# Kernel tuning notes

Hardware: AMD Instinct MI355X
Metric: run time of the kernel (lower is better)

The kernel has to match this reference:

```python
import jax, jax.numpy as jnp
import numpy as np

D_MODEL = 1024
D_HIDDEN = 4096
N_LATENTS = 64
D_LATENT = 1024
N_HEADS = 16
N_EXPERTS = 8
TOP_K = 2
B, T = 2, 2048
D_H = D_LATENT // N_HEADS  # 64


def setup_inputs() -> dict:
    key = jax.random.key(0)
    ks = jax.random.split(key, 16)
    x = jax.random.normal(ks[0], (B, T, D_MODEL), jnp.float32)
    # real RoPE cache (matches RoPE.build_rope_cache)
    half = D_H // 2
    inv_freq = 1.0 / (10000.0 ** (jnp.arange(half, dtype=jnp.float32) / half))
    ang = jnp.arange(T, dtype=jnp.float32)[:, None] * inv_freq[None, :]
    cos, sin = jnp.cos(ang), jnp.sin(ang)
    sL = D_LATENT ** -0.5
    sM = D_MODEL ** -0.5
    sH = D_HIDDEN ** -0.5
    def nrm(k, shape, sc):
        return jax.random.normal(k, shape, jnp.float32) * sc
    aks = jax.random.split(ks[1], 8)
    eks = jax.random.split(ks[2], 3)
    return {
        'x': x, 'cos': cos, 'sin': sin,
        'ln1_g': jnp.ones((D_MODEL,), jnp.float32), 'ln1_b': jnp.zeros((D_MODEL,), jnp.float32),
        'ln2_g': jnp.ones((D_MODEL,), jnp.float32), 'ln2_b': jnp.zeros((D_MODEL,), jnp.float32),
        'ln3_g': jnp.ones((D_MODEL,), jnp.float32), 'ln3_b': jnp.zeros((D_MODEL,), jnp.float32),
        'Lat': nrm(aks[0], (N_LATENTS, D_LATENT), sL),
        'Wq_lat': nrm(aks[1], (D_LATENT, D_LATENT), sL),
        'Wk_in': nrm(aks[2], (D_MODEL, D_LATENT), sM),
        'Wv_in': nrm(aks[3], (D_MODEL, D_LATENT), sM),
        'Wq_in': nrm(aks[4], (D_MODEL, D_LATENT), sM),
        'Wk_lat': nrm(aks[5], (D_LATENT, D_LATENT), sL),
        'Wv_lat': nrm(aks[6], (D_LATENT, D_LATENT), sL),
        'Wout_attn': nrm(aks[7], (D_LATENT, D_MODEL), sL),
        'router_W': nrm(ks[3], (D_MODEL, N_EXPERTS), sM),
        'router_b': jnp.zeros((N_EXPERTS,), jnp.float32),
        'expert_W': nrm(eks[0], (N_EXPERTS, D_MODEL, D_HIDDEN), sM),
        'expert_V': nrm(eks[1], (N_EXPERTS, D_MODEL, D_HIDDEN), sM),
        'expert_Wo': nrm(eks[2], (N_EXPERTS, D_HIDDEN, D_MODEL), sH),
        'lin_W': nrm(ks[4], (D_MODEL, D_MODEL), sM),
        'lin_b': jnp.zeros((D_MODEL,), jnp.float32),
    }


def _layernorm(x, g, b):
    mean = jnp.mean(x, axis=-1, keepdims=True)
    std = jnp.std(x, axis=-1, keepdims=True, ddof=1)  # torch std is unbiased
    return g * (x - mean) / (std + 1e-06) + b


def _split_heads(x):
    b, t, _ = x.shape
    return x.reshape(b, t, N_HEADS, D_H).transpose(0, 2, 1, 3)  # [b,h,t,dh]


def _merge_heads(x):
    b, h, t, dh = x.shape
    return x.transpose(0, 2, 1, 3).reshape(b, t, h * dh)


def _apply_rope(x, cos, sin):
    b, h, s, d = x.shape
    xr = x.reshape(b, h, s, d // 2, 2)
    x1, x2 = xr[..., 0], xr[..., 1]
    c = cos[:s][None, None]
    sn = sin[:s][None, None]
    o1 = x1 * c - x2 * sn
    o2 = x1 * sn + x2 * c
    return jnp.stack([o1, o2], axis=-1).reshape(b, h, s, d)


def _attn(Q, K, V):
    scores = jnp.einsum('bhqd,bhkd->bhqk', Q, K) / (D_H ** 0.5)
    w = jax.nn.softmax(scores, axis=-1)
    return jnp.einsum('bhqk,bhkd->bhqd', w, V)


def _mlha(x, cos, sin, Lat, Wq_lat, Wk_in, Wv_in, Wq_in, Wk_lat, Wv_lat, Wout_attn):
    b = x.shape[0]
    Lb = jnp.broadcast_to(Lat[None], (b, N_LATENTS, D_LATENT))
    Q = _split_heads(Lb @ Wq_lat)
    K = _apply_rope(_split_heads(x @ Wk_in), cos, sin)
    V = _split_heads(x @ Wv_in)
    z = _merge_heads(_attn(Q, K, V))              # [b, n_latents, d_latent]
    Ql = _split_heads(z @ Wq_lat)
    Kl = _split_heads(z @ Wk_lat)
    Vl = _split_heads(z @ Wv_lat)
    z2 = _merge_heads(_attn(Ql, Kl, Vl))          # [b, n_latents, d_latent]
    Qx = _apply_rope(_split_heads(x @ Wq_in), cos, sin)
    Kz = _split_heads(z2 @ Wk_lat)
    Vz = _split_heads(z2 @ Wv_lat)
    xl = _merge_heads(_attn(Qx, Kz, Vz))          # [b, T, d_latent]
    return xl @ Wout_attn


def _moe(x, router_W, router_b, expert_W, expert_V, expert_Wo):
    b, t, d = x.shape
    xf = x.reshape(b * t, d)
    logits = xf @ router_W + router_b                       # [N, E]
    topv, topi = jax.lax.top_k(logits, TOP_K)               # [N, k]
    probs = jax.nn.softmax(topv, axis=-1)                   # [N, k]
    out = jnp.zeros_like(xf)
    for e in range(N_EXPERTS):
        gate = jnp.sum(jnp.where(topi == e, probs, 0.0), axis=-1)  # [N]
        a = xf @ expert_W[e]
        bb = xf @ expert_V[e]
        y = (a * (bb * jax.nn.sigmoid(bb))) @ expert_Wo[e]
        out = out + gate[:, None] * y
    return out.reshape(b, t, d)


def reference(x, cos, sin, ln1_g, ln1_b, ln2_g, ln2_b, ln3_g, ln3_b,
              Lat, Wq_lat, Wk_in, Wv_in, Wq_in, Wk_lat, Wv_lat, Wout_attn,
              router_W, router_b, expert_W, expert_V, expert_Wo, lin_W, lin_b):
    attn = _mlha(x, cos, sin, Lat, Wq_lat, Wk_in, Wv_in, Wq_in, Wk_lat, Wv_lat, Wout_attn)
    x = _layernorm(x, ln1_g, ln1_b) + attn
    x = _layernorm(x, ln2_g, ln2_b) + _moe(x, router_W, router_b, expert_W, expert_V, expert_Wo)
    x = _layernorm(x, ln3_g, ln3_b) + (x @ lin_W + lin_b)
    return x
```

## Files before the change

### kernel.cpp

```cpp
#include <hip/hip_runtime.h>
#include <hip/hip_bf16.h>
#include <math.h>

typedef __hip_bfloat16 bf16;
typedef __attribute__((ext_vector_type(8))) short short8;
typedef __attribute__((ext_vector_type(8))) unsigned short ushort8;
typedef __attribute__((ext_vector_type(4))) float f32x4;

#define NT_   2048
#define NTOK_ 4096
#define DM_   1024
#define DHID_ 4096
#define NEXP_ 8

__device__ __forceinline__ unsigned short f2bf(float f) {
    unsigned u = __float_as_uint(f);
    u = u + 0x7FFF + ((u >> 16) & 1);
    return (unsigned short)(u >> 16);
}

__global__ __launch_bounds__(256) void c2b(const float* __restrict__ in,
        unsigned short* __restrict__ out, int n8)
{
    int i = blockIdx.x * 256 + threadIdx.x;
    if (i >= n8) return;
    const float4 v0 = *(const float4*)(in + (size_t)i * 8);
    const float4 v1 = *(const float4*)(in + (size_t)i * 8 + 4);
    ushort8 o;
    o[0] = f2bf(v0.x); o[1] = f2bf(v0.y); o[2] = f2bf(v0.z); o[3] = f2bf(v0.w);
    o[4] = f2bf(v1.x); o[5] = f2bf(v1.y); o[6] = f2bf(v1.z); o[7] = f2bf(v1.w);
    *(ushort8*)(out + (size_t)i * 8) = o;
}

__global__ __launch_bounds__(256) void tconv(const float* __restrict__ in,
        unsigned short* __restrict__ out, int R, int C)
{
    __shared__ float t[64][65];
    const size_t mofs = (size_t)blockIdx.z * R * C;
    const int r0 = blockIdx.y * 64, c0 = blockIdx.x * 64;
    const int tid = threadIdx.x;
    const int lr = tid >> 4, lc4 = (tid & 15) * 4;
    #pragma unroll
    for (int i = 0; i < 4; ++i) {
        float4 v = *(const float4*)(in + mofs + (size_t)(r0 + lr + i * 16) * C + c0 + lc4);
        t[lr + i * 16][lc4 + 0] = v.x; t[lr + i * 16][lc4 + 1] = v.y;
        t[lr + i * 16][lc4 + 2] = v.z; t[lr + i * 16][lc4 + 3] = v.w;
    }
    __syncthreads();
    const int oc = tid >> 2;
    const int j0 = (tid & 3) * 16;
    ushort8 o0, o1;
    #pragma unroll
    for (int j = 0; j < 8; ++j)  o0[j] = f2bf(t[j0 + j][oc]);
    #pragma unroll
    for (int j = 0; j < 8; ++j)  o1[j] = f2bf(t[j0 + 8 + j][oc]);
    size_t ob = mofs + (size_t)(c0 + oc) * R + r0 + j0;
    *(ushort8*)(out + ob) = o0;
    *(ushort8*)(out + ob + 8) = o1;
}

__global__ __launch_bounds__(256) void tconv3(const float* __restrict__ s0,
        const float* __restrict__ s1, const float* __restrict__ s2,
        unsigned short* __restrict__ out)
{
    __shared__ float t[64][65];
    const float* in = blockIdx.z == 0 ? s0 : (blockIdx.z == 1 ? s1 : s2);
    unsigned short* o = out + (size_t)blockIdx.z * DM_ * DM_;
    const int r0 = blockIdx.y * 64, c0 = blockIdx.x * 64;
    const int tid = threadIdx.x;
    const int lr = tid >> 4, lc4 = (tid & 15) * 4;
    #pragma unroll
    for (int i = 0; i < 4; ++i) {
        float4 v = *(const float4*)(in + (size_t)(r0 + lr + i * 16) * DM_ + c0 + lc4);
        t[lr + i * 16][lc4 + 0] = v.x; t[lr + i * 16][lc4 + 1] = v.y;
        t[lr + i * 16][lc4 + 2] = v.z; t[lr + i * 16][lc4 + 3] = v.w;
    }
    __syncthreads();
    const int oc = tid >> 2;
    const int j0 = (tid & 3) * 16;
    ushort8 o0, o1;
    #pragma unroll
    for (int j = 0; j < 8; ++j)  o0[j] = f2bf(t[j0 + j][oc]);
    #pragma unroll
    for (int j = 0; j < 8; ++j)  o1[j] = f2bf(t[j0 + 8 + j][oc]);
    size_t ob = (size_t)(c0 + oc) * DM_ + r0 + j0;
    *(ushort8*)(o + ob) = o0;
    *(ushort8*)(o + ob + 8) = o1;
}

__global__ __launch_bounds__(256) void tconvEV(const float* __restrict__ s0,
        const float* __restrict__ s1, unsigned short* __restrict__ out)
{
    __shared__ float t[64][65];
    const int z = blockIdx.z;
    const size_t rc = (size_t)DM_ * DHID_;
    const float* in = (z < 8) ? (s0 + (size_t)z * rc) : (s1 + (size_t)(z - 8) * rc);
    unsigned short* o = out + (size_t)z * rc;
    const int r0 = blockIdx.y * 64, c0 = blockIdx.x * 64;
    const int tid = threadIdx.x;
    const int lr = tid >> 4, lc4 = (tid & 15) * 4;
    #pragma unroll
    for (int i = 0; i < 4; ++i) {
        float4 v = *(const float4*)(in + (size_t)(r0 + lr + i * 16) * DHID_ + c0 + lc4);
        t[lr + i * 16][lc4 + 0] = v.x; t[lr + i * 16][lc4 + 1] = v.y;
        t[lr + i * 16][lc4 + 2] = v.z; t[lr + i * 16][lc4 + 3] = v.w;
    }
    __syncthreads();
    const int oc = tid >> 2;
    const int j0 = (tid & 3) * 16;
    ushort8 o0, o1;
    #pragma unroll
    for (int j = 0; j < 8; ++j)  o0[j] = f2bf(t[j0 + j][oc]);
    #pragma unroll
    for (int j = 0; j < 8; ++j)  o1[j] = f2bf(t[j0 + 8 + j][oc]);
    size_t ob = (size_t)(c0 + oc) * DM_ + r0 + j0;
    *(ushort8*)(o + ob) = o0;
    *(ushort8*)(o + ob + 8) = o1;
}

__global__ __launch_bounds__(256) void gemm_bf16_128(
        const unsigned short* __restrict__ A, const unsigned short* __restrict__ BT,
        float* __restrict__ C, int M, int N, int K)
{
    __shared__ unsigned short As[128 * 64];
    __shared__ unsigned short Bs[128 * 64];
    const int tid = threadIdx.x;
    const int wid = tid >> 6, lane = tid & 63;
    const int m0 = blockIdx.y * 128, n0 = blockIdx.x * 128;

    const unsigned short* aSrc[4]; const unsigned short* bSrc[4]; int sWr[4];
    #pragma unroll
    for (int i = 0; i < 4; ++i) {
        int idx = tid + 256 * i;
        int row = idx >> 3, c8 = idx & 7;
        int ar = m0 + row; if (ar >= M) ar = M - 1;
        aSrc[i] = A + (size_t)ar * K + c8 * 8;
        bSrc[i] = BT + (size_t)(n0 + row) * K + c8 * 8;
        sWr[i] = (row * 128 + c8 * 16) ^ ((row & 7) << 4);
    }
    const int wr = wid >> 1, wc = wid & 1;
    int ra[2][4], rb[2][4];
    #pragma unroll
    for (int kk = 0; kk < 2; ++kk) {
        #pragma unroll
        for (int t = 0; t < 4; ++t) {
            int kb = kk * 64 + (lane >> 4) * 16;
            int rowa = wr * 64 + t * 16 + (lane & 15);
            ra[kk][t] = (rowa * 128 + kb) ^ ((rowa & 7) << 4);
            int rowb = wc * 64 + t * 16 + (lane & 15);
            rb[kk][t] = (rowb * 128 + kb) ^ ((rowb & 7) << 4);
        }
    }
    const f32x4 zero = {0.f, 0.f, 0.f, 0.f};
    f32x4 acc[4][4];
    #pragma unroll
    for (int i = 0; i < 4; ++i)
        #pragma unroll
        for (int j = 0; j < 4; ++j) acc[i][j] = zero;

    short8 sa[4], sb[4];
    #pragma unroll
    for (int i = 0; i < 4; ++i) { sa[i] = *(const short8*)(aSrc[i]); sb[i] = *(const short8*)(bSrc[i]); }
    const int nk = K >> 6;
    for (int kt = 0; kt < nk; ++kt) {
        #pragma unroll
        for (int i = 0; i < 4; ++i) {
            *(short8*)((char*)As + sWr[i]) = sa[i];
            *(short8*)((char*)Bs + sWr[i]) = sb[i];
        }
        __syncthreads();
        if (kt + 1 < nk) {
            int ko = (kt + 1) << 6;
            #pragma unroll
            for (int i = 0; i < 4; ++i) { sa[i] = *(const short8*)(aSrc[i] + ko); sb[i] = *(const short8*)(bSrc[i] + ko); }
        }
        #pragma unroll
        for (int kk = 0; kk < 2; ++kk) {
            short8 af[4], bfr[4];
            #pragma unroll
            for (int t = 0; t < 4; ++t) {
                af[t]  = *(const short8*)((const char*)As + ra[kk][t]);
                bfr[t] = *(const short8*)((const char*)Bs + rb[kk][t]);
            }
            #pragma unroll
            for (int i = 0; i < 4; ++i)
                #pragma unroll
                for (int j = 0; j < 4; ++j)
                    acc[i][j] = __builtin_amdgcn_mfma_f32_16x16x32_bf16(af[i], bfr[j], acc[i][j], 0, 0, 0);
        }
        __syncthreads();
    }
    const int cl = lane & 15, g4 = lane >> 4;
    #pragma unroll
    for (int i = 0; i < 4; ++i)
        #pragma unroll
        for (int j = 0; j < 4; ++j)
            #pragma unroll
            for (int r = 0; r < 4; ++r) {
                int rr = m0 + wr * 64 + i * 16 + g4 * 4 + r;
                if (rr < M) C[(size_t)rr * N + n0 + wc * 64 + j * 16 + cl] = acc[i][j][r];
            }
}

__global__ __launch_bounds__(256) void gemm_proj3(
        const unsigned short* __restrict__ A, const unsigned short* __restrict__ BT0,
        float* __restrict__ C0, const float* __restrict__ cosb,
        const float* __restrict__ sinb)
{
    const int z = blockIdx.z;
    const unsigned short* BT = BT0 + (size_t)z * DM_ * DM_;
    float* C = C0 + (size_t)z * NTOK_ * DM_;
    const bool doRope = (z != 1);
    __shared__ unsigned short As[128 * 64];
    __shared__ unsigned short Bs[128 * 64];
    const int tid = threadIdx.x;
    const int wid = tid >> 6, lane = tid & 63;
    const int m0 = blockIdx.y * 128, n0 = blockIdx.x * 128;
    const int K = DM_, N = DM_;

    const unsigned short* aSrc[4]; const unsigned short* bSrc[4]; int sWr[4];
    #pragma unroll
    for (int i = 0; i < 4; ++i) {
        int idx = tid + 256 * i;
        int row = idx >> 3, c8 = idx & 7;
        aSrc[i] = A + (size_t)(m0 + row) * K + c8 * 8;
        bSrc[i] = BT + (size_t)(n0 + row) * K + c8 * 8;
        sWr[i] = (row * 128 + c8 * 16) ^ ((row & 7) << 4);
    }
    const int wr = wid >> 1, wc = wid & 1;
    int ra[2][4], rb[2][4];
    #pragma unroll
    for (int kk = 0; kk < 2; ++kk) {
        #pragma unroll
        for (int t = 0; t < 4; ++t) {
            int kb = kk * 64 + (lane >> 4) * 16;
            int rowa = wr * 64 + t * 16 + (lane & 15);
            ra[kk][t] = (rowa * 128 + kb) ^ ((rowa & 7) << 4);
            int rowb = wc * 64 + t * 16 + (lane & 15);
            rb[kk][t] = (rowb * 128 + kb) ^ ((rowb & 7) << 4);
        }
    }
    const f32x4 zero = {0.f, 0.f, 0.f, 0.f};
    f32x4 acc[4][4];
    #pragma unroll
    for (int i = 0; i < 4; ++i)
        #pragma unroll
        for (int j = 0; j < 4; ++j) acc[i][j] = zero;

    short8 sa[4], sb[4];
    #pragma unroll
    for (int i = 0; i < 4; ++i) { sa[i] = *(const short8*)(aSrc[i]); sb[i] = *(const short8*)(bSrc[i]); }
    const int nk = K >> 6;
    for (int kt = 0; kt < nk; ++kt) {
        #pragma unroll
        for (int i = 0; i < 4; ++i) {
            *(short8*)((char*)As + sWr[i]) = sa[i];
            *(short8*)((char*)Bs + sWr[i]) = sb[i];
        }
        __syncthreads();
        if (kt + 1 < nk) {
            int ko = (kt + 1) << 6;
            #pragma unroll
            for (int i = 0; i < 4; ++i) { sa[i] = *(const short8*)(aSrc[i] + ko); sb[i] = *(const short8*)(bSrc[i] + ko); }
        }
        #pragma unroll
        for (int kk = 0; kk < 2; ++kk) {
            short8 af[4], bfr[4];
            #pragma unroll
            for (int t = 0; t < 4; ++t) {
                af[t]  = *(const short8*)((const char*)As + ra[kk][t]);
                bfr[t] = *(const short8*)((const char*)Bs + rb[kk][t]);
            }
            #pragma unroll
            for (int i = 0; i < 4; ++i)
                #pragma unroll
                for (int j = 0; j < 4; ++j)
                    acc[i][j] = __builtin_amdgcn_mfma_f32_16x16x32_bf16(af[i], bfr[j], acc[i][j], 0, 0, 0);
        }
        __syncthreads();
    }
    const int cl = lane & 15, g4 = lane >> 4;
    #pragma unroll
    for (int i = 0; i < 4; ++i)
        #pragma unroll
        for (int j = 0; j < 4; ++j) {
            const int cc = n0 + wc * 64 + j * 16 + cl;
            const int ii = (cc & 63) >> 1;
            const bool even = (cc & 1) == 0;
            #pragma unroll
            for (int r = 0; r < 4; ++r) {
                const int rr = m0 + wr * 64 + i * 16 + g4 * 4 + r;
                float v = acc[i][j][r];
                float p = __shfl_xor(v, 1, 64);
                float o = v;
                if (doRope) {
                    const int t = rr & (NT_ - 1);
                    float cv = cosb[t * 32 + ii], sv = sinb[t * 32 + ii];
                    o = even ? (v * cv - p * sv) : (p * sv + v * cv);
                }
                C[(size_t)rr * N + cc] = o;
            }
        }
}

__global__ __launch_bounds__(256) void gemm_lat(
        const unsigned short* __restrict__ A, const unsigned short* __restrict__ BT0,
        int btStride, float* __restrict__ C0, int cStride, int M)
{
    const int z = blockIdx.y;
    const unsigned short* BT = BT0 + (size_t)z * btStride;
    float* C = C0 + (size_t)z * cStride;
    const int n0 = blockIdx.x * 64;
    __shared__ unsigned short As[128 * 64];
    __shared__ unsigned short Bs[64 * 64];
    const int tid = threadIdx.x;
    const int wid = tid >> 6, lane = tid & 63;

    const unsigned short* aSrc[4]; int aWr[4];
    #pragma unroll
    for (int i = 0; i < 4; ++i) {
        int idx = tid + 256 * i;
        int row = idx >> 3, c8 = idx & 7;
        int ar = row; if (ar >= M) ar = M - 1;
        aSrc[i] = A + (size_t)ar * DM_ + c8 * 8;
        aWr[i] = (row * 128 + c8 * 16) ^ ((row & 7) << 4);
    }
    const unsigned short* bSrc[2]; int bWr[2];
    #pragma unroll
    for (int i = 0; i < 2; ++i) {
        int idx = tid + 256 * i;
        int row = idx >> 3, c8 = idx & 7;
        bSrc[i] = BT + (size_t)(n0 + row) * DM_ + c8 * 8;
        bWr[i] = (row * 128 + c8 * 16) ^ ((row & 7) << 4);
    }
    const int wr = wid >> 1, wc = wid & 1;
    int ra[2][4], rb[2][2];
    #pragma unroll
    for (int kk = 0; kk < 2; ++kk) {
        #pragma unroll
        for (int t = 0; t < 4; ++t) {
            int rowa = wr * 64 + t * 16 + (lane & 15);
            int kb = kk * 64 + (lane >> 4) * 16;
            ra[kk][t] = (rowa * 128 + kb) ^ ((rowa & 7) << 4);
        }
        #pragma unroll
        for (int t = 0; t < 2; ++t) {
            int rowb = wc * 32 + t * 16 + (lane & 15);
            int kb = kk * 64 + (lane >> 4) * 16;
            rb[kk][t] = (rowb * 128 + kb) ^ ((rowb & 7) << 4);
        }
    }
    const f32x4 zero = {0.f, 0.f, 0.f, 0.f};
    f32x4 acc[4][2];
    #pragma unroll
    for (int i = 0; i < 4; ++i)
        #pragma unroll
        for (int j = 0; j < 2; ++j) acc[i][j] = zero;

    short8 sa[4], sb[2];
    #pragma unroll
    for (int i = 0; i < 4; ++i) sa[i] = *(const short8*)(aSrc[i]);
    #pragma unroll
    for (int i = 0; i < 2; ++i) sb[i] = *(const short8*)(bSrc[i]);
    const int nk = DM_ >> 6;
    for (int kt = 0; kt < nk; ++kt) {
        #pragma unroll
        for (int i = 0; i < 4; ++i) *(short8*)((char*)As + aWr[i]) = sa[i];
        #pragma unroll
        for (int i = 0; i < 2; ++i) *(short8*)((char*)Bs + bWr[i]) = sb[i];
        __syncthreads();
        if (kt + 1 < nk) {
            int ko = (kt + 1) << 6;
            #pragma unroll
            for (int i = 0; i < 4; ++i) sa[i] = *(const short8*)(aSrc[i] + ko);
            #pragma unroll
            for (int i = 0; i < 2; ++i) sb[i] = *(const short8*)(bSrc[i] + ko);
        }
        #pragma unroll
        for (int kk = 0; kk < 2; ++kk) {
            short8 af[4], bf2[2];
            #pragma unroll
            for (int t = 0; t < 4; ++t) af[t] = *(const short8*)((const char*)As + ra[kk][t]);
            #pragma unroll
            for (int t = 0; t < 2; ++t) bf2[t] = *(const short8*)((const char*)Bs + rb[kk][t]);
            #pragma unroll
            for (int i = 0; i < 4; ++i)
                #pragma unroll
                for (int j = 0; j < 2; ++j)
                    acc[i][j] = __builtin_amdgcn_mfma_f32_16x16x32_bf16(af[i], bf2[j], acc[i][j], 0, 0, 0);
        }
        __syncthreads();
    }
    const int cl = lane & 15, g4 = lane >> 4;
    #pragma unroll
    for (int i = 0; i < 4; ++i)
        #pragma unroll
        for (int j = 0; j < 2; ++j)
            #pragma unroll
            for (int r = 0; r < 4; ++r) {
                int rl = wr * 64 + i * 16 + g4 * 4 + r;
                if (rl < M)
                    C[(size_t)rl * DM_ + n0 + wc * 32 + j * 16 + cl] = acc[i][j][r];
            }
}

__global__ __launch_bounds__(256) void attn_scores(float* __restrict__ S,
        const float* __restrict__ Q, const float* __restrict__ Km,
        int M, int T, int q_bs, int k_bs, float scale)
{
    const int bh = blockIdx.z, b = bh >> 4, h = bh & 15;
    const int t0 = blockIdx.x * 64, q0 = blockIdx.y * 64;
    __shared__ float Qs[64][65], Ks[64][65];
    const int tid = threadIdx.x;
    const int lr = tid >> 2, lc = (tid & 3) * 16;
    {
        int q = q0 + lr;
        if (q < M) {
            const float* Qp = Q + ((size_t)q_bs * b + q) * DM_ + h * 64 + lc;
            #pragma unroll
            for (int j = 0; j < 16; ++j) Qs[lr][lc + j] = Qp[j];
        } else {
            #pragma unroll
            for (int j = 0; j < 16; ++j) Qs[lr][lc + j] = 0.f;
        }
        const float* Kp = Km + ((size_t)k_bs * b + t0 + lr) * DM_ + h * 64 + lc;
        #pragma unroll
        for (int j = 0; j < 16; ++j) Ks[lr][lc + j] = Kp[j];
    }
    __syncthreads();
    const int ty = tid >> 4, tx = tid & 15;
    float acc[4][4] = {};
    for (int d = 0; d < 64; ++d) {
        float a[4], kk[4];
        #pragma unroll
        for (int i = 0; i < 4; ++i) a[i] = Qs[ty * 4 + i][d];
        #pragma unroll
        for (int j = 0; j < 4; ++j) kk[j] = Ks[tx * 4 + j][d];
        #pragma unroll
        for (int i = 0; i < 4; ++i)
            #pragma unroll
            for (int j = 0; j < 4; ++j) acc[i][j] += a[i] * kk[j];
    }
    #pragma unroll
    for (int i = 0; i < 4; ++i) {
        int q = q0 + ty * 4 + i;
        if (q < M) {
            float* Sp = S + ((size_t)bh * M + q) * T + t0 + tx * 4;
            #pragma unroll
            for (int j = 0; j < 4; ++j) Sp[j] = acc[i][j] * scale;
        }
    }
}

__global__ __launch_bounds__(256) void softmax_rows(float* __restrict__ S, int L)
{
    float* p = S + (size_t)blockIdx.x * L;
    const int tid = threadIdx.x;
    __shared__ float red[256];
    float m = -1e30f;
    for (int i = tid; i < L; i += 256) m = fmaxf(m, p[i]);
    red[tid] = m; __syncthreads();
    for (int s = 128; s; s >>= 1) { if (tid < s) red[tid] = fmaxf(red[tid], red[tid + s]); __syncthreads(); }
    m = red[0]; __syncthreads();
    float sum = 0.f;
    for (int i = tid; i < L; i += 256) { float e = __expf(p[i] - m); p[i] = e; sum += e; }
    red[tid] = sum; __syncthreads();
    for (int s = 128; s; s >>= 1) { if (tid < s) red[tid] += red[tid + s]; __syncthreads(); }
    float inv = 1.f / red[0];
    for (int i = tid; i < L; i += 256) p[i] *= inv;
}

__global__ __launch_bounds__(256) void fused_attn64(unsigned short* __restrict__ Ob,
        const float* __restrict__ Q, const float* __restrict__ Kp,
        const float* __restrict__ Vp, int q_bs)
{
    const int bh = blockIdx.y, b = bh >> 4, h = bh & 15;
    const int q0 = blockIdx.x * 64;
    __shared__ float Qs[64][65], Ks[64][65], Vs[64][65];
    __shared__ float ls[64];
    const int tid = threadIdx.x;
    const int lr = tid >> 2, lc = (tid & 3) * 16;
    {
        const float* Qr = Q + ((size_t)q_bs * b + q0 + lr) * DM_ + h * 64 + lc;
        #pragma unroll
        for (int j = 0; j < 16; ++j) Qs[lr][lc + j] = Qr[j];
        const float* Kr = Kp + ((size_t)64 * b + lr) * DM_ + h * 64 + lc;
        #pragma unroll
        for (int j = 0; j < 16; ++j) Ks[lr][lc + j] = Kr[j];
        const float* Vr = Vp + ((size_t)64 * b + lr) * DM_ + h * 64 + lc;
        #pragma unroll
        for (int j = 0; j < 16; ++j) Vs[lr][lc + j] = Vr[j];
    }
    __syncthreads();
    const int ty = tid >> 4, tx = tid & 15;
    float acc[4][4] = {};
    for (int d = 0; d < 64; ++d) {
        float a[4], kk[4];
        #pragma unroll
        for (int i = 0; i < 4; ++i) a[i] = Qs[ty * 4 + i][d];
        #pragma unroll
        for (int j = 0; j < 4; ++j) kk[j] = Ks[tx * 4 + j][d];
        #pragma unroll
        for (int i = 0; i < 4; ++i)
            #pragma unroll
            for (int j = 0; j < 4; ++j) acc[i][j] += a[i] * kk[j];
    }
    float p[4][4]; float lsum[4];
    #pragma unroll
    for (int i = 0; i < 4; ++i) {
        float m = fmaxf(fmaxf(acc[i][0], acc[i][1]), fmaxf(acc[i][2], acc[i][3]));
        #pragma unroll
        for (int o = 1; o <= 8; o <<= 1) m = fmaxf(m, __shfl_xor(m, o, 64));
        float s = 0.f;
        #pragma unroll
        for (int j = 0; j < 4; ++j) { p[i][j] = __expf(acc[i][j] * 0.125f - m * 0.125f); s += p[i][j]; }
        #pragma unroll
        for (int o = 1; o <= 8; o <<= 1) s += __shfl_xor(s, o, 64);
        lsum[i] = s;
    }
    __syncthreads();
    #pragma unroll
    for (int i = 0; i < 4; ++i) {
        #pragma unroll
        for (int j = 0; j < 4; ++j) Qs[ty * 4 + i][tx * 4 + j] = p[i][j];
        if (tx == 0) ls[ty * 4 + i] = lsum[i];
    }
    __syncthreads();
    float O[4][4] = {};
    for (int t = 0; t < 64; ++t) {
        float pp[4], vv[4];
        #pragma unroll
        for (int i = 0; i < 4; ++i) pp[i] = Qs[ty * 4 + i][t];
        #pragma unroll
        for (int j = 0; j < 4; ++j) vv[j] = Vs[t][tx * 4 + j];
        #pragma unroll
        for (int i = 0; i < 4; ++i)
            #pragma unroll
            for (int j = 0; j < 4; ++j) O[i][j] += pp[i] * vv[j];
    }
    #pragma unroll
    for (int i = 0; i < 4; ++i) {
        float inv = 1.f / ls[ty * 4 + i];
        size_t ofs = ((size_t)q_bs * b + q0 + ty * 4 + i) * DM_ + h * 64 + tx * 4;
        #pragma unroll
        for (int j = 0; j < 4; ++j) Ob[ofs + j] = f2bf(O[i][j] * inv);
    }
}

__global__ __launch_bounds__(256) void pv_split(float* __restrict__ part,
        const float* __restrict__ P, const float* __restrict__ V)
{
    const int c = blockIdx.x, bh = blockIdx.y, b = bh >> 4, h = bh & 15;
    __shared__ float Ps[64][65], Vs[64][65];
    const int tid = threadIdx.x;
    const int lr = tid >> 2, lc = (tid & 3) * 16;
    const int ty = tid >> 4, tx = tid & 15;
    float acc[4][4] = {};
    for (int it = 0; it < 4; ++it) {
        const int t0 = c * 256 + it * 64;
        const float* Pp = P + ((size_t)bh * 64 + lr) * NT_ + t0 + lc;
        #pragma unroll
        for (int j = 0; j < 16; ++j) Ps[lr][lc + j] = Pp[j];
        const float* Vp = V + ((size_t)NT_ * b + t0 + lr) * DM_ + h * 64 + lc;
        #pragma unroll
        for (int j = 0; j < 16; ++j) Vs[lr][lc + j] = Vp[j];
        __syncthreads();
        for (int t = 0; t < 64; ++t) {
            float pp[4], vv[4];
            #pragma unroll
            for (int i = 0; i < 4; ++i) pp[i] = Ps[ty * 4 + i][t];
            #pragma unroll
            for (int j = 0; j < 4; ++j) vv[j] = Vs[t][tx * 4 + j];
            #pragma unroll
            for (int i = 0; i < 4; ++i)
                #pragma unroll
                for (int j = 0; j < 4; ++j) acc[i][j] += pp[i] * vv[j];
        }
        __syncthreads();
    }
    float* op = part + ((size_t)bh * 8 + c) * 4096;
    #pragma unroll
    for (int i = 0; i < 4; ++i)
        #pragma unroll
        for (int j = 0; j < 4; ++j)
            op[(ty * 4 + i) * 64 + tx * 4 + j] = acc[i][j];
}

__global__ __launch_bounds__(256) void pv_combine(const float* __restrict__ part,
        unsigned short* __restrict__ Zb)
{
    const int bh = blockIdx.x, b = bh >> 4, h = bh & 15;
    for (int idx = threadIdx.x; idx < 4096; idx += 256) {
        int q = idx >> 6, d = idx & 63;
        float s = 0.f;
        #pragma unroll
        for (int c = 0; c < 8; ++c) s += part[((size_t)bh * 8 + c) * 4096 + idx];
        Zb[(size_t)(b * 64 + q) * DM_ + h * 64 + d] = f2bf(s);
    }
}

__global__ __launch_bounds__(256) void ln_add_dual(const float* __restrict__ X,
        const float* __restrict__ g, const float* __restrict__ bb,
        const float* __restrict__ add, float* __restrict__ out,
        unsigned short* __restrict__ outb)
{
    const int n = blockIdx.x, tid = threadIdx.x;
    const float* x = X + (size_t)n * DM_;
    __shared__ float red[256];
    float v[4]; float s = 0.f;
    #pragma unroll
    for (int i = 0; i < 4; ++i) { v[i] = x[tid + i * 256]; s += v[i]; }
    red[tid] = s; __syncthreads();
    for (int st = 128; st; st >>= 1) { if (tid < st) red[tid] += red[tid + st]; __syncthreads(); }
    float mean = red[0] * (1.f / 1024.f);
    __syncthreads();
    float vs = 0.f;
    #pragma unroll
    for (int i = 0; i < 4; ++i) { float d = v[i] - mean; vs += d * d; }
    red[tid] = vs; __syncthreads();
    for (int st = 128; st; st >>= 1) { if (tid < st) red[tid] += red[tid + st]; __syncthreads(); }
    float inv = 1.f / (sqrtf(red[0] * (1.f / 1023.f)) + 1e-6f);
    #pragma unroll
    for (int i = 0; i < 4; ++i) {
        int d = tid + i * 256;
        float r = g[d] * (v[i] - mean) * inv + bb[d] + add[(size_t)n * DM_ + d];
        out[(size_t)n * DM_ + d] = r;
        outb[(size_t)n * DM_ + d] = f2bf(r);
    }
}

__global__ __launch_bounds__(256) void ln_final(const float* __restrict__ X,
        const float* __restrict__ g, const float* __restrict__ bb,
        const float* __restrict__ t, const float* __restrict__ lb,
        float* __restrict__ out)
{
    const int n = blockIdx.x, tid = threadIdx.x;
    const float* x = X + (size_t)n * DM_;
    __shared__ float red[256];
    float v[4]; float s = 0.f;
    #pragma unroll
    for (int i = 0; i < 4; ++i) { v[i] = x[tid + i * 256]; s += v[i]; }
    red[tid] = s; __syncthreads();
    for (int st = 128; st; st >>= 1) { if (tid < st) red[tid] += red[tid + st]; __syncthreads(); }
    float mean = red[0] * (1.f / 1024.f);
    __syncthreads();
    float vs = 0.f;
    #pragma unroll
    for (int i = 0; i < 4; ++i) { float d = v[i] - mean; vs += d * d; }
    red[tid] = vs; __syncthreads();
    for (int st = 128; st; st >>= 1) { if (tid < st) red[tid] += red[tid + st]; __syncthreads(); }
    float inv = 1.f / (sqrtf(red[0] * (1.f / 1023.f)) + 1e-6f);
    #pragma unroll
    for (int i = 0; i < 4; ++i) {
        int d = tid + i * 256;
        out[(size_t)n * DM_ + d] = g[d] * (v[i] - mean) * inv + bb[d]
                                 + t[(size_t)n * DM_ + d] + lb[d];
    }
}

__global__ __launch_bounds__(256) void router_kernel(const float* __restrict__ X1,
        const float* __restrict__ Wr, const float* __restrict__ br,
        int* __restrict__ topi, float* __restrict__ gates, int* __restrict__ counts)
{
    const int n = blockIdx.x, tid = threadIdx.x;
    const int e = tid >> 5, l = tid & 31;
    const float* x = X1 + (size_t)n * DM_;
    float s = 0.f;
    for (int k = l; k < DM_; k += 32) s += x[k] * Wr[k * NEXP_ + e];
    for (int off = 16; off; off >>= 1) s += __shfl_down(s, off, 32);
    __shared__ float lg[NEXP_];
    if (l == 0) lg[e] = s + br[e];
    __syncthreads();
    if (tid == 0) {
        float v1 = -1e30f; int i1 = 0;
        for (int ee = 0; ee < NEXP_; ++ee) if (lg[ee] > v1) { v1 = lg[ee]; i1 = ee; }
        float v2 = -1e30f; int i2 = 0;
        for (int ee = 0; ee < NEXP_; ++ee) if (ee != i1 && lg[ee] > v2) { v2 = lg[ee]; i2 = ee; }
        float e2 = __expf(v2 - v1);
        float inv = 1.f / (1.f + e2);
        topi[n * 2] = i1; topi[n * 2 + 1] = i2;
        gates[n * 2] = inv; gates[n * 2 + 1] = e2 * inv;
        atomicAdd(&counts[i1], 1); atomicAdd(&counts[i2], 1);
    }
}

__global__ void zero_counts(int* __restrict__ counts)
{
    if (threadIdx.x < NEXP_) counts[threadIdx.x] = 0;
}

__global__ void router_offsets(const int* __restrict__ counts, int* __restrict__ offs,
                               int* __restrict__ fill)
{
    if (threadIdx.x == 0) {
        int acc = 0;
        for (int e = 0; e < NEXP_; ++e) { offs[e] = acc; acc += counts[e]; fill[e] = 0; }
    }
}

__global__ __launch_bounds__(256) void router_scatter(const int* __restrict__ topi,
        int* __restrict__ fill, const int* __restrict__ offs,
        int* __restrict__ ptok, int* __restrict__ pidx)
{
    int n = blockIdx.x * 256 + threadIdx.x;
    if (n >= NTOK_) return;
    #pragma unroll
    for (int s2 = 0; s2 < 2; ++s2) {
        int e = topi[n * 2 + s2];
        int r = atomicAdd(&fill[e], 1);
        int p = offs[e] + r;
        ptok[p] = n;
        pidx[n * 2 + s2] = p;
    }
}

__global__ __launch_bounds__(256) void moe_up_mfma(
        const unsigned short* __restrict__ X1b,
        const unsigned short* __restrict__ WTa, const unsigned short* __restrict__ VTa,
        unsigned short* __restrict__ H,
        const int* __restrict__ cnt, const int* __restrict__ offs,
        const int* __restrict__ ptok)
{
    const int e = blockIdx.z;
    const int ce = cnt[e];
    const int m0 = blockIdx.y * 128;
    if (m0 >= ce) return;
    const int n0 = blockIdx.x * 64;
    const int base = offs[e];
    const unsigned short* WT = WTa + (size_t)e * DHID_ * DM_;
    const unsigned short* VT = VTa + (size_t)e * DHID_ * DM_;
    __shared__ unsigned short As[128 * 64];
    __shared__ unsigned short Ws[64 * 64];
    __shared__ unsigned short Vs[64 * 64];
    __shared__ int rtok[128];
    const int tid = threadIdx.x;
    const int wid = tid >> 6, lane = tid & 63;
    if (tid < 128) {
        int r = m0 + tid;
        rtok[tid] = (r < ce) ? ptok[base + r] : ptok[base + ce - 1];
    }
    __syncthreads();

    const unsigned short* aSrc[4]; int aWr[4];
    #pragma unroll
    for (int i = 0; i < 4; ++i) {
        int idx = tid + 256 * i;
        int row = idx >> 3, c8 = idx & 7;
        aSrc[i] = X1b + (size_t)rtok[row] * DM_ + c8 * 8;
        aWr[i] = (row * 128 + c8 * 16) ^ ((row & 7) << 4);
    }
    const unsigned short* wSrc[2]; const unsigned short* vSrc[2]; int bWr[2];
    #pragma unroll
    for (int i = 0; i < 2; ++i) {
        int idx = tid + 256 * i;
        int row = idx >> 3, c8 = idx & 7;
        wSrc[i] = WT + (size_t)(n0 + row) * DM_ + c8 * 8;
        vSrc[i] = VT + (size_t)(n0 + row) * DM_ + c8 * 8;
        bWr[i] = (row * 128 + c8 * 16) ^ ((row & 7) << 4);
    }
    const int wr = wid >> 1, wc = wid & 1;
    int ra[2][4], rb[2][2];
    #pragma unroll
    for (int kk = 0; kk < 2; ++kk) {
        #pragma unroll
        for (int t = 0; t < 4; ++t) {
            int rowa = wr * 64 + t * 16 + (lane & 15);
            int kb = kk * 64 + (lane >> 4) * 16;
            ra[kk][t] = (rowa * 128 + kb) ^ ((rowa & 7) << 4);
        }
        #pragma unroll
        for (int t = 0; t < 2; ++t) {
            int rowb = wc * 32 + t * 16 + (lane & 15);
            int kb = kk * 64 + (lane >> 4) * 16;
            rb[kk][t] = (rowb * 128 + kb) ^ ((rowb & 7) << 4);
        }
    }
    const f32x4 zero = {0.f, 0.f, 0.f, 0.f};
    f32x4 accw[4][2], accv[4][2];
    #pragma unroll
    for (int i = 0; i < 4; ++i)
        #pragma unroll
        for (int j = 0; j < 2; ++j) { accw[i][j] = zero; accv[i][j] = zero; }

    short8 sa[4], sw[2], sv[2];
    #pragma unroll
    for (int i = 0; i < 4; ++i) sa[i] = *(const short8*)(aSrc[i]);
    #pragma unroll
    for (int i = 0; i < 2; ++i) { sw[i] = *(const short8*)(wSrc[i]); sv[i] = *(const short8*)(vSrc[i]); }
    const int nk = DM_ >> 6;
    for (int kt = 0; kt < nk; ++kt) {
        #pragma unroll
        for (int i = 0; i < 4; ++i) *(short8*)((char*)As + aWr[i]) = sa[i];
        #pragma unroll
        for (int i = 0; i < 2; ++i) {
            *(short8*)((char*)Ws + bWr[i]) = sw[i];
            *(short8*)((char*)Vs + bWr[i]) = sv[i];
        }
        __syncthreads();
        if (kt + 1 < nk) {
            int ko = (kt + 1) << 6;
            #pragma unroll
            for (int i = 0; i < 4; ++i) sa[i] = *(const short8*)(aSrc[i] + ko);
            #pragma unroll
            for (int i = 0; i < 2; ++i) { sw[i] = *(const short8*)(wSrc[i] + ko); sv[i] = *(const short8*)(vSrc[i] + ko); }
        }
        #pragma unroll
        for (int kk = 0; kk < 2; ++kk) {
            short8 af[4], bw[2], bv[2];
            #pragma unroll
            for (int t = 0; t < 4; ++t) af[t] = *(const short8*)((const char*)As + ra[kk][t]);
            #pragma unroll
            for (int t = 0; t < 2; ++t) {
                bw[t] = *(const short8*)((const char*)Ws + rb[kk][t]);
                bv[t] = *(const short8*)((const char*)Vs + rb[kk][t]);
            }
            #pragma unroll
            for (int i = 0; i < 4; ++i)
                #pragma unroll
                for (int j = 0; j < 2; ++j) {
                    accw[i][j] = __builtin_amdgcn_mfma_f32_16x16x32_bf16(af[i], bw[j], accw[i][j], 0, 0, 0);
                    accv[i][j] = __builtin_amdgcn_mfma_f32_16x16x32_bf16(af[i], bv[j], accv[i][j], 0, 0, 0);
                }
        }
        __syncthreads();
    }
    const int cl = lane & 15, g4 = lane >> 4;
    #pragma unroll
    for (int i = 0; i < 4; ++i)
        #pragma unroll
        for (int j = 0; j < 2; ++j)
            #pragma unroll
            for (int r = 0; r < 4; ++r) {
                int rl = m0 + wr * 64 + i * 16 + g4 * 4 + r;
                if (rl < ce) {
                    float a = accw[i][j][r], b = accv[i][j][r];
                    float h = a * (b / (1.f + __expf(-b)));
                    H[(size_t)(base + rl) * DHID_ + n0 + wc * 32 + j * 16 + cl] = f2bf(h);
                }
            }
}

__global__ __launch_bounds__(256) void moe_down_mfma(
        const unsigned short* __restrict__ H, const unsigned short* __restrict__ WoTa,
        float* __restrict__ PY,
        const int* __restrict__ cnt, const int* __restrict__ offs)
{
    const int e = blockIdx.z;
    const int ce = cnt[e];
    const int m0 = blockIdx.y * 128;
    if (m0 >= ce) return;
    const int n0 = blockIdx.x * 128;
    const int base = offs[e];
    const unsigned short* WoT = WoTa + (size_t)e * DM_ * DHID_;
    __shared__ unsigned short As[128 * 64];
    __shared__ unsigned short Bs[128 * 64];
    const int tid = threadIdx.x;
    const int wid = tid >> 6, lane = tid & 63;

    const unsigned short* aSrc[4]; const unsigned short* bSrc[4]; int sWr[4];
    #pragma unroll
    for (int i = 0; i < 4; ++i) {
        int idx = tid + 256 * i;
        int row = idx >> 3, c8 = idx & 7;
        int r = m0 + row; if (r >= ce) r = ce - 1;
        aSrc[i] = H + (size_t)(base + r) * DHID_ + c8 * 8;
        bSrc[i] = WoT + (size_t)(n0 + row) * DHID_ + c8 * 8;
        sWr[i] = (row * 128 + c8 * 16) ^ ((row & 7) << 4);
    }
    const int wr = wid >> 1, wc = wid & 1;
    int ra[2][4], rb[2][4];
    #pragma unroll
    for (int kk = 0; kk < 2; ++kk) {
        #pragma unroll
        for (int t = 0; t < 4; ++t) {
            int kb = kk * 64 + (lane >> 4) * 16;
            int rowa = wr * 64 + t * 16 + (lane & 15);
            ra[kk][t] = (rowa * 128 + kb) ^ ((rowa & 7) << 4);
            int rowb = wc * 64 + t * 16 + (lane & 15);
            rb[kk][t] = (rowb * 128 + kb) ^ ((rowb & 7) << 4);
        }
    }
    const f32x4 zero = {0.f, 0.f, 0.f, 0.f};
    f32x4 acc[4][4];
    #pragma unroll
    for (int i = 0; i < 4; ++i)
        #pragma unroll
        for (int j = 0; j < 4; ++j) acc[i][j] = zero;

    short8 sa[4], sb[4];
    #pragma unroll
    for (int i = 0; i < 4; ++i) { sa[i] = *(const short8*)(aSrc[i]); sb[i] = *(const short8*)(bSrc[i]); }
    const int nk = DHID_ >> 6;
    for (int kt = 0; kt < nk; ++kt) {
        #pragma unroll
        for (int i = 0; i < 4; ++i) {
            *(short8*)((char*)As + sWr[i]) = sa[i];
            *(short8*)((char*)Bs + sWr[i]) = sb[i];
        }
        __syncthreads();
        if (kt + 1 < nk) {
            int ko = (kt + 1) << 6;
            #pragma unroll
            for (int i = 0; i < 4; ++i) { sa[i] = *(const short8*)(aSrc[i] + ko); sb[i] = *(const short8*)(bSrc[i] + ko); }
        }
        #pragma unroll
        for (int kk = 0; kk < 2; ++kk) {
            short8 af[4], bfr[4];
            #pragma unroll
            for (int t = 0; t < 4; ++t) {
                af[t]  = *(const short8*)((const char*)As + ra[kk][t]);
                bfr[t] = *(const short8*)((const char*)Bs + rb[kk][t]);
            }
            #pragma unroll
            for (int i = 0; i < 4; ++i)
                #pragma unroll
                for (int j = 0; j < 4; ++j)
                    acc[i][j] = __builtin_amdgcn_mfma_f32_16x16x32_bf16(af[i], bfr[j], acc[i][j], 0, 0, 0);
        }
        __syncthreads();
    }
    const int cl = lane & 15, g4 = lane >> 4;
    #pragma unroll
    for (int i = 0; i < 4; ++i)
        #pragma unroll
        for (int j = 0; j < 4; ++j)
            #pragma unroll
            for (int r = 0; r < 4; ++r) {
                int rl = m0 + wr * 64 + i * 16 + g4 * 4 + r;
                if (rl < ce)
                    PY[(size_t)(base + rl) * DM_ + n0 + wc * 64 + j * 16 + cl] = acc[i][j][r];
            }
}

__global__ __launch_bounds__(256) void moe_combine(const float* __restrict__ PY,
        const int* __restrict__ pidx, const float* __restrict__ gates,
        float* __restrict__ MO)
{
    int n = blockIdx.x, tid = threadIdx.x;
    int p0 = pidx[n * 2], p1 = pidx[n * 2 + 1];
    float g0 = gates[n * 2], g1 = gates[n * 2 + 1];
    #pragma unroll
    for (int i = 0; i < 4; ++i) {
        int d = tid + i * 256;
        MO[(size_t)n * DM_ + d] = g0 * PY[(size_t)p0 * DM_ + d] + g1 * PY[(size_t)p1 * DM_ + d];
    }
}

extern "C" void kernel_launch(void* const* d_in, const int* in_sizes, int n_in,
                              void* d_out, int out_size, void* d_ws, size_t ws_size,
                              hipStream_t stream)
{
    const float* x      = (const float*)d_in[0];
    const float* cosb   = (const float*)d_in[1];
    const float* sinb   = (const float*)d_in[2];
    const float* ln1g   = (const float*)d_in[3];
    const float* ln1b   = (const float*)d_in[4];
    const float* ln2g   = (const float*)d_in[5];
    const float* ln2b   = (const float*)d_in[6];
    const float* ln3g   = (const float*)d_in[7];
    const float* ln3b   = (const float*)d_in[8];
    const float* Lat    = (const float*)d_in[9];
    const float* Wq_lat = (const float*)d_in[10];
    const float* Wk_in  = (const float*)d_in[11];
    const float* Wv_in  = (const float*)d_in[12];
    const float* Wq_in  = (const float*)d_in[13];
    const float* Wk_lat = (const float*)d_in[14];
    const float* Wv_lat = (const float*)d_in[15];
    const float* Wout   = (const float*)d_in[16];
    const float* rW     = (const float*)d_in[17];
    const float* rb     = (const float*)d_in[18];
    const float* eW     = (const float*)d_in[19];
    const float* eV     = (const float*)d_in[20];
    const float* eWo    = (const float*)d_in[21];
    const float* linW   = (const float*)d_in[22];
    const float* linb   = (const float*)d_in[23];
    float* out = (float*)d_out;

    float* ws = (float*)d_ws;
    const size_t M1 = 1024 * 1024;
    float* buf0 = ws;
    float* buf1 = ws + 4 * M1;
    float* buf2 = ws + 8 * M1;
    float* buf3 = ws + 12 * M1;
    size_t off = 16 * M1;
    float* qlat = ws + off; off += 65536;
    float* qlb  = ws + off; off += 131072;
    float* klb  = ws + off; off += 131072;
    float* vlb  = ws + off; off += 131072;
    float* s2b  = ws + off; off += 131072;
    float* z2b  = ws + off; off += 131072;
    float* kzb  = ws + off; off += 131072;
    float* vzb  = ws + off; off += 131072;
    float* gates = ws + off; off += 8192;
    int* iarea = (int*)(ws + off); off += 32768;
    int* topi   = iarea;
    int* counts = iarea + 8192;
    int* offs   = iarea + 8200;
    int* fill   = iarea + 8208;
    int* ptok   = iarea + 8216;
    int* pidx   = iarea + 16408;
    unsigned short* zb_b  = (unsigned short*)(ws + off); off += 65536;
    unsigned short* z2b_b = (unsigned short*)(ws + off); off += 65536;
    unsigned short* latb  = (unsigned short*)(ws + off); off += 32768;
    unsigned short* x1b   = (unsigned short*)(ws + off); off += 2 * M1;
    unsigned short* WkT   = (unsigned short*)(ws + off); off += 3 * (M1 / 2);
    unsigned short* WoutT = (unsigned short*)(ws + off); off += M1 / 2;
    unsigned short* linWT = (unsigned short*)(ws + off); off += M1 / 2;
    unsigned short* WlatT = (unsigned short*)(ws + off); off += 3 * (M1 / 2);

    unsigned short* Hbuf  = (unsigned short*)(ws + 24 * M1);
    unsigned short* actb  = (unsigned short*)(ws + 24 * M1);
    unsigned short* x2b   = (unsigned short*)(ws + 24 * M1);
    float* pvpart         = ws + 26 * M1;
    unsigned short* eWT   = (unsigned short*)(ws + 40 * M1);
    unsigned short* eVT   = (unsigned short*)(ws + 56 * M1);
    unsigned short* eWoT  = eWT;
    float* PY             = ws + 56 * M1;

    dim3 blk(256);

    zero_counts<<<1, 64, 0, stream>>>(counts);

    tconv3<<<dim3(16, 16, 3), blk, 0, stream>>>(Wk_in, Wv_in, Wq_in, WkT);
    tconv3<<<dim3(16, 16, 2), blk, 0, stream>>>(Wout, linW, linW, WoutT);
    tconv3<<<dim3(16, 16, 3), blk, 0, stream>>>(Wq_lat, Wk_lat, Wv_lat, WlatT);
    tconvEV<<<dim3(64, 16, 16), blk, 0, stream>>>(eW, eV, eWT);
    c2b<<<2048, blk, 0, stream>>>(x, actb, 524288);
    c2b<<<32, blk, 0, stream>>>(Lat, latb, 8192);

    gemm_lat<<<dim3(16, 1), blk, 0, stream>>>(latb, WlatT, (int)M1, qlat, 0, 64);

    gemm_proj3<<<dim3(8, 32, 3), blk, 0, stream>>>(actb, WkT, buf0, cosb, sinb);

    attn_scores<<<dim3(32, 1, 32), blk, 0, stream>>>(buf3, qlat, buf0, 64, 2048, 0, 2048, 0.125f);
    softmax_rows<<<2048, blk, 0, stream>>>(buf3, 2048);
    pv_split<<<dim3(8, 32), blk, 0, stream>>>(pvpart, buf3, buf1);
    pv_combine<<<32, blk, 0, stream>>>(pvpart, zb_b);

    gemm_lat<<<dim3(16, 3), blk, 0, stream>>>(zb_b, WlatT, (int)M1, qlb, 131072, 128);
    fused_attn64<<<dim3(1, 32), blk, 0, stream>>>(z2b_b, qlb, klb, vlb, 64);

    gemm_lat<<<dim3(16, 2), blk, 0, stream>>>(z2b_b, WlatT + M1, (int)M1, kzb, 131072, 128);
    fused_attn64<<<dim3(32, 32), blk, 0, stream>>>(actb, buf2, kzb, vzb, 2048);
    gemm_bf16_128<<<dim3(8, 32), blk, 0, stream>>>(actb, WoutT, buf1, 4096, 1024, 1024);

    ln_add_dual<<<4096, blk, 0, stream>>>(x, ln1g, ln1b, buf1, buf2, x1b);

    router_kernel<<<4096, blk, 0, stream>>>(buf2, rW, rb, topi, gates, counts);
    router_offsets<<<1, 64, 0, stream>>>(counts, offs, fill);
    router_scatter<<<16, blk, 0, stream>>>(topi, fill, offs, ptok, pidx);
    moe_up_mfma<<<dim3(64, 32, 8), blk, 0, stream>>>(x1b, eWT, eVT, Hbuf, counts, offs, ptok);
    tconv<<<dim3(16, 64, 8), blk, 0, stream>>>(eWo, eWoT, 4096, 1024);
    moe_down_mfma<<<dim3(8, 32, 8), blk, 0, stream>>>(Hbuf, eWoT, PY, counts, offs);
    moe_combine<<<4096, blk, 0, stream>>>(PY, pidx, gates, buf0);

    ln_add_dual<<<4096, blk, 0, stream>>>(buf2, ln2g, ln2b, buf0, buf1, x2b);

    gemm_bf16_128<<<dim3(8, 32), blk, 0, stream>>>(x2b, linWT, buf3, 4096, 1024, 1024);
    ln_final<<<4096, blk, 0, stream>>>(buf1, ln3g, ln3b, buf3, linb, out);
}
```

Baseline: 993.5 us.

## Register-cache softmax rows, split pv_combine over more blocks, store MoE outputs as bf16

The softmax kernel is specialised to rows of 2048 and keeps each row's values in registers, so the score matrix is read once and written once instead of being read three times. pv_combine now runs on 8x more blocks so more of the GPU is busy. The MoE down-projection writes per-expert outputs as bf16 instead of fp32, halving the PY write and the gather reads in moe_combine. The bf16 intermediate adds rounding error to the MoE output.

New measurement: 982.7 us. About the same (-1.1%).

```diff
diff --git a/kernel.cpp b/kernel.cpp
--- a/kernel.cpp
+++ b/kernel.cpp
@@ -17,6 +17,9 @@
     unsigned u = __float_as_uint(f);
     u = u + 0x7FFF + ((u >> 16) & 1);
     return (unsigned short)(u >> 16);
+}
+__device__ __forceinline__ float bf2f(unsigned short u) {
+    return __uint_as_float((unsigned)u << 16);
 }
 
 __global__ __launch_bounds__(256) void c2b(const float* __restrict__ in,
@@ -452,22 +455,26 @@
     }
 }
 
-__global__ __launch_bounds__(256) void softmax_rows(float* __restrict__ S, int L)
-{
-    float* p = S + (size_t)blockIdx.x * L;
+__global__ __launch_bounds__(256) void softmax_rows2048(float* __restrict__ S)
+{
+    float* p = S + (size_t)blockIdx.x * 2048;
     const int tid = threadIdx.x;
     __shared__ float red[256];
+    float v[8];
     float m = -1e30f;
-    for (int i = tid; i < L; i += 256) m = fmaxf(m, p[i]);
+    #pragma unroll
+    for (int i = 0; i < 8; ++i) { v[i] = p[tid + i * 256]; m = fmaxf(m, v[i]); }
     red[tid] = m; __syncthreads();
     for (int s = 128; s; s >>= 1) { if (tid < s) red[tid] = fmaxf(red[tid], red[tid + s]); __syncthreads(); }
     m = red[0]; __syncthreads();
     float sum = 0.f;
-    for (int i = tid; i < L; i += 256) { float e = __expf(p[i] - m); p[i] = e; sum += e; }
+    #pragma unroll
+    for (int i = 0; i < 8; ++i) { v[i] = __expf(v[i] - m); sum += v[i]; }
     red[tid] = sum; __syncthreads();
     for (int s = 128; s; s >>= 1) { if (tid < s) red[tid] += red[tid + s]; __syncthreads(); }
     float inv = 1.f / red[0];
-    for (int i = tid; i < L; i += 256) p[i] *= inv;
+    #pragma unroll
+    for (int i = 0; i < 8; ++i) p[tid + i * 256] = v[i] * inv;
 }
 
 __global__ __launch_bounds__(256) void fused_attn64(unsigned short* __restrict__ Ob,
@@ -590,7 +597,9 @@
         unsigned short* __restrict__ Zb)
 {
     const int bh = blockIdx.x, b = bh >> 4, h = bh & 15;
-    for (int idx = threadIdx.x; idx < 4096; idx += 256) {
+    const int seg = blockIdx.y;
+    for (int k = 0; k < 2; ++k) {
+        int idx = seg * 512 + k * 256 + threadIdx.x;
         int q = idx >> 6, d = idx & 63;
         float s = 0.f;
         #pragma unroll
@@ -842,7 +851,7 @@
 
 __global__ __launch_bounds__(256) void moe_down_mfma(
         const unsigned short* __restrict__ H, const unsigned short* __restrict__ WoTa,
-        float* __restrict__ PY,
+        unsigned short* __restrict__ PY,
         const int* __restrict__ cnt, const int* __restrict__ offs)
 {
     const int e = blockIdx.z;
@@ -928,11 +937,11 @@
             for (int r = 0; r < 4; ++r) {
                 int rl = m0 + wr * 64 + i * 16 + g4 * 4 + r;
                 if (rl < ce)
-                    PY[(size_t)(base + rl) * DM_ + n0 + wc * 64 + j * 16 + cl] = acc[i][j][r];
+                    PY[(size_t)(base + rl) * DM_ + n0 + wc * 64 + j * 16 + cl] = f2bf(acc[i][j][r]);
             }
 }
 
-__global__ __launch_bounds__(256) void moe_combine(const float* __restrict__ PY,
+__global__ __launch_bounds__(256) void moe_combine(const unsigned short* __restrict__ PY,
         const int* __restrict__ pidx, const float* __restrict__ gates,
         float* __restrict__ MO)
 {
@@ -942,7 +951,8 @@
     #pragma unroll
     for (int i = 0; i < 4; ++i) {
         int d = tid + i * 256;
-        MO[(size_t)n * DM_ + d] = g0 * PY[(size_t)p0 * DM_ + d] + g1 * PY[(size_t)p1 * DM_ + d];
+        MO[(size_t)n * DM_ + d] = g0 * bf2f(PY[(size_t)p0 * DM_ + d])
+                                + g1 * bf2f(PY[(size_t)p1 * DM_ + d]);
     }
 }
 
@@ -1015,7 +1025,7 @@
     unsigned short* eWT   = (unsigned short*)(ws + 40 * M1);
     unsigned short* eVT   = (unsigned short*)(ws + 56 * M1);
     unsigned short* eWoT  = eWT;
-    float* PY             = ws + 56 * M1;
+    unsigned short* PY    = (unsigned short*)(ws + 56 * M1);
 
     dim3 blk(256);
 
@@ -1033,9 +1043,9 @@
     gemm_proj3<<<dim3(8, 32, 3), blk, 0, stream>>>(actb, WkT, buf0, cosb, sinb);
 
     attn_scores<<<dim3(32, 1, 32), blk, 0, stream>>>(buf3, qlat, buf0, 64, 2048, 0, 2048, 0.125f);
-    softmax_rows<<<2048, blk, 0, stream>>>(buf3, 2048);
+    softmax_rows2048<<<2048, blk, 0, stream>>>(buf3);
     pv_split<<<dim3(8, 32), blk, 0, stream>>>(pvpart, buf3, buf1);
-    pv_combine<<<32, blk, 0, stream>>>(pvpart, zb_b);
+    pv_combine<<<dim3(32, 8), blk, 0, stream>>>(pvpart, zb_b);
 
     gemm_lat<<<dim3(16, 3), blk, 0, stream>>>(zb_b, WlatT, (int)M1, qlb, 131072, 128);
     fused_attn64<<<dim3(1, 32), blk, 0, stream>>>(z2b_b, qlb, klb, vlb, 64);
```
